# Kernel optimization log

Hardware: AMD Instinct MI355X
Metric: run time of the kernel (lower is better)

The kernel has to match this reference:

```python
import jax, jax.numpy as jnp
import numpy as np
from jax import lax

EPS = 1e-6


def layernorm2d(x, w, b):
    # channel LayerNorm over dim C of NCHW (biased variance), matching LayerNormFunction
    mu = jnp.mean(x, axis=1, keepdims=True)
    var = jnp.mean((x - mu) ** 2, axis=1, keepdims=True)
    y = (x - mu) * lax.rsqrt(var + EPS)
    return w[None, :, None, None] * y + b[None, :, None, None]


def conv1x1(x, W, b):
    # x: (N,C,H,W), W: (O,C), b: (O,)
    return jnp.einsum('nchw,oc->nohw', x, W) + b[None, :, None, None]


def conv3x3(x, W, b):
    # W: (O,I,3,3)
    y = lax.conv_general_dilated(x, W, window_strides=(1, 1), padding='SAME',
                                 dimension_numbers=('NCHW', 'OIHW', 'NCHW'))
    return y + b[None, :, None, None]


def avg_pool3x3(x):
    # torch F.avg_pool2d k=3, s=1, p=1, count_include_pad=True -> always divide by 9
    s = lax.reduce_window(x, 0.0, lax.add, (1, 1, 3, 3), (1, 1, 1, 1),
                          [(0, 0), (0, 0), (1, 1), (1, 1)])
    return s / 9.0


def setup_inputs() -> dict:
    key = jax.random.key(0)
    N, C, H, W = 8, 64, 128, 256
    ks = jax.random.split(key, 12)
    d = {
        'x_l': jax.random.normal(ks[0], (N, C, H, W), jnp.float32),
        'x_r': jax.random.normal(ks[1], (N, C, H, W), jnp.float32),
        'nl_w': jnp.ones((C,), jnp.float32),
        'nl_b': jnp.zeros((C,), jnp.float32),
        'nr_w': jnp.ones((C,), jnp.float32),
        'nr_b': jnp.zeros((C,), jnp.float32),
        'Wq_l': jax.random.normal(ks[2], (C, C), jnp.float32) * 0.05,
        'bq_l': jax.random.normal(ks[3], (C,), jnp.float32) * 0.05,
        'Wq_r': jax.random.normal(ks[4], (C, C), jnp.float32) * 0.05,
        'bq_r': jax.random.normal(ks[5], (C,), jnp.float32) * 0.05,
        'Wv_r': jax.random.normal(ks[6], (C, C), jnp.float32) * 0.05,
        'bv_r': jax.random.normal(ks[7], (C,), jnp.float32) * 0.05,
        'beta': jax.random.normal(ks[8], (1, C, 1, 1), jnp.float32) * 0.1,
        'gamma': jax.random.normal(ks[9], (1, C, 1, 1), jnp.float32) * 0.1,
        'W_hf': jax.random.normal(ks[10], (C, C, 3, 3), jnp.float32) * 0.02,
        'b_hf': jax.random.normal(ks[11], (C,), jnp.float32) * 0.02,
    }
    return d


def reference(x_l, x_r, nl_w, nl_b, nr_w, nr_b, Wq_l, bq_l, Wq_r, bq_r,
              Wv_r, bv_r, beta, gamma, W_hf, b_hf):
    C = x_l.shape[1]
    scale = C ** (-0.5)

    # Projections (1x1 convs); Q_l, Q_r, V_r as (N,H,W,C)
    Q_l = jnp.transpose(conv1x1(layernorm2d(x_l, nl_w, nl_b), Wq_l, bq_l), (0, 2, 3, 1))
    Q_r = jnp.transpose(conv1x1(layernorm2d(x_r, nr_w, nr_b), Wq_r, bq_r), (0, 2, 3, 1))
    V_r = jnp.transpose(conv1x1(x_r, Wv_r, bv_r), (0, 2, 3, 1))

    # Per-scanline cross attention: (N,H,W,W)
    attn = jnp.einsum('nhwc,nhvc->nhwv', Q_l, Q_r) * scale
    attn = jax.nn.softmax(attn, axis=-1)
    F_r2l = jnp.einsum('nhwv,nhvc->nhwc', attn, V_r)  # (N,H,W,C)
    F_r2l = jnp.transpose(F_r2l, (0, 3, 1, 2)) * beta  # (N,C,H,W)

    # High-frequency branch
    hf = conv3x3(x_r - avg_pool3x3(x_r), W_hf, b_hf)

    return x_l + F_r2l + gamma * hf
```

## Files before the change

### kernel.cpp

```cpp
#include <hip/hip_runtime.h>
#include <hip/hip_bf16.h>

#define N_ 8
#define C_ 64
#define H_ 128
#define W_ 256
#define HW_ (H_*W_)
#define CHW_ (C_*H_*W_)

typedef unsigned int u32;
typedef unsigned short u16;
typedef float f32x4 __attribute__((ext_vector_type(4)));
typedef short bf16x8 __attribute__((ext_vector_type(8)));

__device__ __forceinline__ float blo(u32 u) { return __uint_as_float(u << 16); }
__device__ __forceinline__ float bhi(u32 u) { return __uint_as_float(u & 0xffff0000u); }
__device__ __forceinline__ u16 f2bf(float f) {
    u32 u = __float_as_uint(f);
    u32 lsb = (u >> 16) & 1u;
    u += 0x7fffu + lsb;
    return (u16)(u >> 16);
}
__device__ __forceinline__ u32 pack2(float a, float b) {
    return (u32)f2bf(a) | ((u32)f2bf(b) << 16);
}
__device__ __forceinline__ int rmap(int px) {
    return (px & 0xF8) | ((px + (px >> 3)) & 7);
}

__global__ __launch_bounds__(512, 2) void k_fused(
    const float* __restrict__ xl, const float* __restrict__ xr,
    const float* __restrict__ nlw, const float* __restrict__ nlb,
    const float* __restrict__ nrw, const float* __restrict__ nrb,
    const float* __restrict__ Wql, const float* __restrict__ bql,
    const float* __restrict__ Wqr, const float* __restrict__ bqr,
    const float* __restrict__ Wvr, const float* __restrict__ bvr,
    const float* __restrict__ beta, float* __restrict__ out)
{
    __shared__ u32 B1[8192];
    __shared__ u32 B2[8192];
    __shared__ float muA[256], rsA[256];
    __shared__ float SlA[64], BlA[64], SrA[64], BrA[64], BvA[64];
    const int tid  = threadIdx.x;
    const int lane = tid & 63, wv = tid >> 6;
    const int l15  = lane & 15, kg = lane >> 4;
    const int mw   = wv & 3;
    const int nh   = wv >> 2;
    const int blk  = blockIdx.x;
    const int n = blk >> 7, h = blk & 127;
    const size_t gbase = (size_t)n*CHW_ + (size_t)h*W_;

    if (tid < 64) {
        const int o = tid;
        float sl = 0.f, bl = bql[o], sr = 0.f, br = bqr[o];
        for (int c = 0; c < 64; ++c) {
            float wl = Wql[o*64+c], wr = Wqr[o*64+c];
            sl += wl * nlw[c];
            bl += wl * nlb[c];
            sr += wr * nrw[c];
            br += wr * nrb[c];
        }
        SlA[o] = sl; BlA[o] = bl; SrA[o] = sr; BrA[o] = br; BvA[o] = bvr[o];
    }

    const int oA = mw*16 + l15;
    bf16x8 aL[2], aR[2], aV[2];
    #pragma unroll
    for (int hf = 0; hf < 2; ++hf) {
        bf16x8 tl, tr, tv;
        #pragma unroll
        for (int j = 0; j < 8; ++j) {
            const int c = hf*32 + kg*8 + j;
            tl[j] = (short)f2bf(Wql[oA*64+c] * nlw[c]);
            tr[j] = (short)f2bf(Wqr[oA*64+c] * nrw[c]);
            tv[j] = (short)f2bf(Wvr[oA*64+c]);
        }
        aL[hf] = tl; aR[hf] = tr; aV[hf] = tv;
    }

    {
        const int chunk = tid >> 6;
        const int j = tid & 63;
        const int c0 = chunk*8;
        float4 v[8];
        #pragma unroll
        for (int e = 0; e < 8; ++e)
            v[e] = *(const float4*)(xl + gbase + (size_t)(c0+e)*HW_ + j*4);
        #pragma unroll
        for (int t = 0; t < 4; ++t) {
            const int px = j*4 + t;
            const int r = rmap(px);
            u32 q0,q1,q2,q3;
            const float* f0 = (const float*)&v[0]; const float* f1 = (const float*)&v[1];
            const float* f2 = (const float*)&v[2]; const float* f3 = (const float*)&v[3];
            const float* f4 = (const float*)&v[4]; const float* f5 = (const float*)&v[5];
            const float* f6 = (const float*)&v[6]; const float* f7 = (const float*)&v[7];
            asm("v_cvt_pk_bf16_f32 %0, %1, %2" : "=v"(q0) : "v"(f0[t]), "v"(f1[t]));
            asm("v_cvt_pk_bf16_f32 %0, %1, %2" : "=v"(q1) : "v"(f2[t]), "v"(f3[t]));
            asm("v_cvt_pk_bf16_f32 %0, %1, %2" : "=v"(q2) : "v"(f4[t]), "v"(f5[t]));
            asm("v_cvt_pk_bf16_f32 %0, %1, %2" : "=v"(q3) : "v"(f6[t]), "v"(f7[t]));
            uint4 pv; pv.x=q0; pv.y=q1; pv.z=q2; pv.w=q3;
            *(uint4*)&B1[r*32 + ((chunk ^ (r&7))<<2)] = pv;
        }
    }
    __syncthreads();
    if (tid < 256) {
        const int px = tid;
        const int r = rmap(px);
        float sum = 0.f, ssq = 0.f;
        #pragma unroll
        for (int c8 = 0; c8 < 8; ++c8) {
            uint4 val = *(const uint4*)&B1[r*32 + ((c8 ^ (r&7))<<2)];
            const u32* wp = (const u32*)&val;
            #pragma unroll
            for (int q = 0; q < 4; ++q) {
                float a = blo(wp[q]), b = bhi(wp[q]);
                sum += a + b; ssq += a*a + b*b;
            }
        }
        float mu = sum * (1.f/64.f);
        float var = ssq * (1.f/64.f) - mu*mu;
        muA[px] = mu;
        rsA[px] = rsqrtf(var + 1e-6f);
    }
    __syncthreads();
    {
        float Sv[4], Bv[4];
        #pragma unroll
        for (int r4 = 0; r4 < 4; ++r4) {
            Sv[r4] = SlA[mw*16 + kg*4 + r4];
            Bv[r4] = BlA[mw*16 + kg*4 + r4];
        }
        #pragma unroll
        for (int nt2 = 0; nt2 < 8; ++nt2) {
            const int nt = nh*8 + nt2;
            const int px = nt*16 + l15;
            const int r = rmap(px);
            f32x4 d = {0.f,0.f,0.f,0.f};
            #pragma unroll
            for (int hf = 0; hf < 2; ++hf) {
                bf16x8 b = *(const bf16x8*)&B1[r*32 + (((hf*4+kg) ^ (r&7))<<2)];
                d = __builtin_amdgcn_mfma_f32_16x16x32_bf16(aL[hf], b, d, 0, 0, 0);
            }
            const float mu = muA[px], rs = rsA[px];
            uint2 pv;
            pv.x = pack2(rs*(d[0] - mu*Sv[0]) + Bv[0], rs*(d[1] - mu*Sv[1]) + Bv[1]);
            pv.y = pack2(rs*(d[2] - mu*Sv[2]) + Bv[2], rs*(d[3] - mu*Sv[3]) + Bv[3]);
            const int ci = (mw*2 + (kg>>1)) ^ (px & 7);
            *(uint2*)&B2[px*32 + (ci<<2) + (kg&1)*2] = pv;
        }
    }
    __syncthreads();

    bf16x8 qf[2][2];
    #pragma unroll
    for (int ntq = 0; ntq < 2; ++ntq)
        #pragma unroll
        for (int ci = 0; ci < 2; ++ci) {
            const int q = wv*32 + ntq*16 + l15;
            qf[ntq][ci] = *(const bf16x8*)&B2[q*32 + (((ci*4+kg) ^ (q&7))<<2)];
        }
    {
        const int chunk = tid >> 6;
        const int j = tid & 63;
        const int c0 = chunk*8;
        float4 v[8];
        #pragma unroll
        for (int e = 0; e < 8; ++e)
            v[e] = *(const float4*)(xr + gbase + (size_t)(c0+e)*HW_ + j*4);
        #pragma unroll
        for (int t = 0; t < 4; ++t) {
            const int px = j*4 + t;
            const int r = rmap(px);
            u32 q0,q1,q2,q3;
            const float* f0 = (const float*)&v[0]; const float* f1 = (const float*)&v[1];
            const float* f2 = (const float*)&v[2]; const float* f3 = (const float*)&v[3];
            const float* f4 = (const float*)&v[4]; const float* f5 = (const float*)&v[5];
            const float* f6 = (const float*)&v[6]; const float* f7 = (const float*)&v[7];
            asm("v_cvt_pk_bf16_f32 %0, %1, %2" : "=v"(q0) : "v"(f0[t]), "v"(f1[t]));
            asm("v_cvt_pk_bf16_f32 %0, %1, %2" : "=v"(q1) : "v"(f2[t]), "v"(f3[t]));
            asm("v_cvt_pk_bf16_f32 %0, %1, %2" : "=v"(q2) : "v"(f4[t]), "v"(f5[t]));
            asm("v_cvt_pk_bf16_f32 %0, %1, %2" : "=v"(q3) : "v"(f6[t]), "v"(f7[t]));
            uint4 pv; pv.x=q0; pv.y=q1; pv.z=q2; pv.w=q3;
            *(uint4*)&B1[r*32 + ((chunk ^ (r&7))<<2)] = pv;
        }
    }
    __syncthreads();
    if (tid < 256) {
        const int px = tid;
        const int r = rmap(px);
        float sum = 0.f, ssq = 0.f;
        #pragma unroll
        for (int c8 = 0; c8 < 8; ++c8) {
            uint4 val = *(const uint4*)&B1[r*32 + ((c8 ^ (r&7))<<2)];
            const u32* wp = (const u32*)&val;
            #pragma unroll
            for (int q = 0; q < 4; ++q) {
                float a = blo(wp[q]), b = bhi(wp[q]);
                sum += a + b; ssq += a*a + b*b;
            }
        }
        float mu = sum * (1.f/64.f);
        float var = ssq * (1.f/64.f) - mu*mu;
        muA[px] = mu;
        rsA[px] = rsqrtf(var + 1e-6f);
    }
    __syncthreads();

    u32 hq[8][2], hv[8][2];
    {
        float Sv[4], Bv[4];
        #pragma unroll
        for (int r4 = 0; r4 < 4; ++r4) {
            Sv[r4] = SrA[mw*16 + kg*4 + r4];
            Bv[r4] = BrA[mw*16 + kg*4 + r4];
        }
        const int chv = mw*16 + l15;
        const float vbias = BvA[chv];
        #pragma unroll
        for (int nt2 = 0; nt2 < 8; ++nt2) {
            const int nt = nh*8 + nt2;
            const int px = nt*16 + l15;
            const int r = rmap(px);
            bf16x8 bX[2];
            #pragma unroll
            for (int hf = 0; hf < 2; ++hf)
                bX[hf] = *(const bf16x8*)&B1[r*32 + (((hf*4+kg) ^ (r&7))<<2)];
            f32x4 dq = {0.f,0.f,0.f,0.f};
            f32x4 dv = {0.f,0.f,0.f,0.f};
            #pragma unroll
            for (int hf = 0; hf < 2; ++hf) {
                dq = __builtin_amdgcn_mfma_f32_16x16x32_bf16(aR[hf], bX[hf], dq, 0, 0, 0);
                dv = __builtin_amdgcn_mfma_f32_16x16x32_bf16(bX[hf], aV[hf], dv, 0, 0, 0);
            }
            const float mu = muA[px], rs = rsA[px];
            hq[nt2][0] = pack2(rs*(dq[0] - mu*Sv[0]) + Bv[0], rs*(dq[1] - mu*Sv[1]) + Bv[1]);
            hq[nt2][1] = pack2(rs*(dq[2] - mu*Sv[2]) + Bv[2], rs*(dq[3] - mu*Sv[3]) + Bv[3]);
            hv[nt2][0] = pack2(dv[0] + vbias, dv[1] + vbias);
            hv[nt2][1] = pack2(dv[2] + vbias, dv[3] + vbias);
        }
    }
    __syncthreads();
    {
        const int chv = mw*16 + l15;
        u16* Vts16 = (u16*)B2;
        #pragma unroll
        for (int nt2 = 0; nt2 < 8; ++nt2) {
            const int nt = nh*8 + nt2;
            const int px = nt*16 + l15;
            const int ciq = (mw*2 + (kg>>1)) ^ (px & 7);
            uint2 pq; pq.x = hq[nt2][0]; pq.y = hq[nt2][1];
            *(uint2*)&B1[px*32 + (ciq<<2) + (kg&1)*2] = pq;
            uint2 pw; pw.x = hv[nt2][0]; pw.y = hv[nt2][1];
            const int swz = (nt*2 + (kg>>1)) ^ (chv & 7);
            *(uint2*)&Vts16[chv*256 + (swz<<3) + (kg&1)*4] = pw;
        }
    }
    __syncthreads();

    f32x4 oacc[2][4];
    #pragma unroll
    for (int a = 0; a < 2; ++a)
        #pragma unroll
        for (int b = 0; b < 4; ++b)
            oacc[a][b] = (f32x4){0.f,0.f,0.f,0.f};
    float lsum[2] = {0.f,0.f};
    const uint4* KsR = (const uint4*)B1;
    const u16* Vts = (const u16*)B2;
    const int srcA = ((2*kg) & 3)*16 + l15;

    for (int kb = 0; kb < 8; ++kb) {
        f32x4 st[2][2];
        #pragma unroll
        for (int mt = 0; mt < 2; ++mt)
            #pragma unroll
            for (int nt = 0; nt < 2; ++nt)
                st[mt][nt] = (f32x4){0.f,0.f,0.f,0.f};
        #pragma unroll
        for (int ci = 0; ci < 2; ++ci) {
            bf16x8 a0 = *(const bf16x8*)&KsR[(kb*32 +      l15)*8 + ((ci*4 + kg) ^ (l15 & 7))];
            bf16x8 a1 = *(const bf16x8*)&KsR[(kb*32 + 16 + l15)*8 + ((ci*4 + kg) ^ (l15 & 7))];
            #pragma unroll
            for (int nt = 0; nt < 2; ++nt) {
                st[0][nt] = __builtin_amdgcn_mfma_f32_16x16x32_bf16(a0, qf[nt][ci], st[0][nt], 0, 0, 0);
                st[1][nt] = __builtin_amdgcn_mfma_f32_16x16x32_bf16(a1, qf[nt][ci], st[1][nt], 0, 0, 0);
            }
        }
        bf16x8 paR[2];
        #pragma unroll
        for (int nt = 0; nt < 2; ++nt) {
            float p00 = __expf(st[0][nt][0]*0.125f);
            float p01 = __expf(st[0][nt][1]*0.125f);
            float p02 = __expf(st[0][nt][2]*0.125f);
            float p03 = __expf(st[0][nt][3]*0.125f);
            float p10 = __expf(st[1][nt][0]*0.125f);
            float p11 = __expf(st[1][nt][1]*0.125f);
            float p12 = __expf(st[1][nt][2]*0.125f);
            float p13 = __expf(st[1][nt][3]*0.125f);
            lsum[nt] += ((p00+p01)+(p02+p03)) + ((p10+p11)+(p12+p13));
            u32 pk00, pk01, pk10, pk11;
            asm("v_cvt_pk_bf16_f32 %0, %1, %2" : "=v"(pk00) : "v"(p00), "v"(p01));
            asm("v_cvt_pk_bf16_f32 %0, %1, %2" : "=v"(pk01) : "v"(p02), "v"(p03));
            asm("v_cvt_pk_bf16_f32 %0, %1, %2" : "=v"(pk10) : "v"(p10), "v"(p11));
            asm("v_cvt_pk_bf16_f32 %0, %1, %2" : "=v"(pk11) : "v"(p12), "v"(p13));
            int a00 = __shfl((int)pk00, srcA, 64);
            int a01 = __shfl((int)pk01, srcA, 64);
            int a10 = __shfl((int)pk10, srcA, 64);
            int a11 = __shfl((int)pk11, srcA, 64);
            int b00 = __shfl((int)pk00, srcA + 16, 64);
            int b01 = __shfl((int)pk01, srcA + 16, 64);
            int b10 = __shfl((int)pk10, srcA + 16, 64);
            int b11 = __shfl((int)pk11, srcA + 16, 64);
            const bool lo = (kg < 2);
            union { u32 u[4]; bf16x8 v; } pu;
            pu.u[0] = (u32)(lo ? a00 : a10);
            pu.u[1] = (u32)(lo ? a01 : a11);
            pu.u[2] = (u32)(lo ? b00 : b10);
            pu.u[3] = (u32)(lo ? b01 : b11);
            paR[nt] = pu.v;
        }
        bf16x8 vb[4];
        #pragma unroll
        for (int nc = 0; nc < 4; ++nc)
            vb[nc] = *(const bf16x8*)&Vts[(nc*16 + l15)*256 + ((kb*4 + kg) ^ (l15 & 7))*8];
        #pragma unroll
        for (int qt = 0; qt < 2; ++qt)
            #pragma unroll
            for (int nc = 0; nc < 4; ++nc)
                oacc[qt][nc] = __builtin_amdgcn_mfma_f32_16x16x32_bf16(paR[qt], vb[nc], oacc[qt][nc], 0, 0, 0);
    }

    #pragma unroll
    for (int nt = 0; nt < 2; ++nt) {
        float s = lsum[nt];
        s += __shfl_xor(s, 16, 64);
        s += __shfl_xor(s, 32, 64);
        lsum[nt] = s;
    }
    float linv[2][4];
    #pragma unroll
    for (int qt = 0; qt < 2; ++qt)
        #pragma unroll
        for (int r = 0; r < 4; ++r)
            linv[qt][r] = 1.0f / __shfl(lsum[qt], kg*4 + r, 64);

    const size_t qbase = gbase + wv*32;
    #pragma unroll
    for (int nc = 0; nc < 4; ++nc) {
        const int ch = nc*16 + l15;
        const float bch = beta[ch];
        #pragma unroll
        for (int qt = 0; qt < 2; ++qt) {
            const size_t gidx = qbase + (size_t)ch*HW_ + qt*16 + kg*4;
            f32x4 x4 = *(const f32x4*)&xl[gidx];
            f32x4 vals;
            #pragma unroll
            for (int r = 0; r < 4; ++r)
                vals[r] = x4[r] + bch*(oacc[qt][nc][r]*linv[qt][r]);
            *(f32x4*)&out[gidx] = vals;
        }
    }
}

__global__ __launch_bounds__(256) void k_hipass(
    const float* __restrict__ xr, u16* __restrict__ Tt)
{
    __shared__ u16 Ts[64*256];
    const int bid = blockIdx.x;
    const int blk = (bid & 7)*128 + (bid >> 3);
    const int n = blk >> 7, h = blk & 127;
    const int tid = threadIdx.x;
    const int lane = tid & 63, wv = tid >> 6;
    const float* rowp = xr + (size_t)n*CHW_ + (size_t)h*W_ + lane*4;

    #pragma unroll
    for (int ci = 0; ci < 16; ++ci) {
        const int c = wv*16 + ci;
        const float* pc = rowp + (size_t)c*HW_;
        float ctr0=0.f, ctr1=0.f, ctr2=0.f, ctr3=0.f;
        float s0=0.f, s1=0.f, s2=0.f, s3=0.f;
        #pragma unroll
        for (int dy = -1; dy <= 1; ++dy) {
            const int hh = h + dy;
            float4 v = {0.f,0.f,0.f,0.f};
            if (hh >= 0 && hh < 128) v = *(const float4*)(pc + dy*W_);
            float lft = __shfl_up(v.w, 1);
            float rgt = __shfl_down(v.x, 1);
            if (lane == 0)  lft = 0.f;
            if (lane == 63) rgt = 0.f;
            s0 += lft + v.x + v.y;
            s1 += v.x + v.y + v.z;
            s2 += v.y + v.z + v.w;
            s3 += v.z + v.w + rgt;
            if (dy == 0) { ctr0=v.x; ctr1=v.y; ctr2=v.z; ctr3=v.w; }
        }
        uint2 pv;
        pv.x = pack2(ctr0 - s0*(1.f/9.f), ctr1 - s1*(1.f/9.f));
        pv.y = pack2(ctr2 - s2*(1.f/9.f), ctr3 - s3*(1.f/9.f));
        const int swz = (c >> 3) << 3;
        *(uint2*)&Ts[c*256 + ((lane*4) ^ swz)] = pv;
    }
    __syncthreads();
    uint4* gout = (uint4*)(Tt + (size_t)blk*256*64);
    #pragma unroll
    for (int iter = 0; iter < 8; ++iter) {
        const int lin = iter*256 + tid;
        const int px = lin >> 3, chunk = lin & 7;
        const int pxs = px ^ (chunk << 3);
        u32 w4[4];
        #pragma unroll
        for (int tp = 0; tp < 4; ++tp) {
            const int c0 = chunk*8 + tp*2;
            u16 a = Ts[(c0    )*256 + pxs];
            u16 b = Ts[(c0 + 1)*256 + pxs];
            w4[tp] = (u32)a | ((u32)b << 16);
        }
        uint4 v; v.x=w4[0]; v.y=w4[1]; v.z=w4[2]; v.w=w4[3];
        gout[lin] = v;
    }
}

__device__ __forceinline__ void conv_tile(
    const uint4* __restrict__ buf, const bf16x8* A,
    const float* gv, const float* bv,
    int n, int h, int w0, int mt, int l15, int kg,
    float* __restrict__ out)
{
    f32x4 acc[4] = {{0,0,0,0},{0,0,0,0},{0,0,0,0},{0,0,0,0}};
    #pragma unroll
    for (int s = 0; s < 18; ++s) {
        const int q  = s >> 1;
        const int dy = q / 3, dx = q % 3;
        const int c0 = (s & 1)*4 + kg;
        #pragma unroll
        for (int nt = 0; nt < 4; ++nt) {
            const int wt = nt*16 + l15 + dx;
            bf16x8 b = *(const bf16x8*)&buf[(dy*66 + wt)*8 + (c0 ^ (wt & 7))];
            acc[nt] = __builtin_amdgcn_mfma_f32_16x16x32_bf16(A[s], b, acc[nt], 0, 0, 0);
        }
    }
    #pragma unroll
    for (int nt = 0; nt < 4; ++nt) {
        const int px = w0 + nt*16 + l15;
        #pragma unroll
        for (int r = 0; r < 4; ++r) {
            const int oo = mt*16 + kg*4 + r;
            size_t idx = (size_t)(n*64 + oo)*HW_ + (size_t)h*W_ + px;
            out[idx] += gv[r]*(acc[nt][r] + bv[r]);
        }
    }
}

__global__ __launch_bounds__(256) void k_conv(
    const u16* __restrict__ Tt, const float* __restrict__ Whf,
    const float* __restrict__ bhf, const float* __restrict__ gam,
    float* __restrict__ out)
{
    __shared__ uint4 Xs[2][1584];
    const int tid  = threadIdx.x;
    const int lane = tid & 63;
    const int mt   = tid >> 6;
    const int l15  = lane & 15;
    const int kg   = lane >> 4;
    const int bid  = blockIdx.x;
    const int blk2 = (bid & 7)*256 + (bid >> 3);
    const int row  = blk2 >> 1, half = blk2 & 1;
    const int n = row >> 7, h = row & 127;
    const int w00 = half*128;
    const int w01 = w00 + 64;

    const int oa = mt*16 + l15;
    bf16x8 A[18];
    #pragma unroll
    for (int s = 0; s < 18; ++s) {
        const int q  = s >> 1;
        const int ib = (s & 1)*32 + kg*8;
        bf16x8 a;
        #pragma unroll
        for (int j = 0; j < 8; ++j) {
            float wv = Whf[(size_t)(oa*64 + ib + j)*9 + q];
            a[j] = (short)f2bf(wv);
        }
        A[s] = a;
    }
    float gv[4], bv[4];
    #pragma unroll
    for (int r = 0; r < 4; ++r) {
        int oo = mt*16 + kg*4 + r;
        gv[r] = gam[oo];
        bv[r] = bhf[oo];
    }

    for (int it = tid; it < 1584; it += 256) {
        int dy    = it / 528;
        int rem   = it - dy*528;
        int wt    = rem >> 3;
        int chunk = rem & 7;
        int hh = h + dy - 1;
        int wg = w00 + wt - 1;
        uint4 v = {0,0,0,0};
        if (hh >= 0 && hh < 128 && wg >= 0 && wg < 256)
            v = *(const uint4*)(Tt + (((size_t)(n*128 + hh)*256 + wg)*64 + chunk*8));
        Xs[0][(dy*66 + wt)*8 + (chunk ^ (wt & 7))] = v;
    }
    __syncthreads();

    uint4 rr[7];
    #pragma unroll
    for (int k = 0; k < 7; ++k) {
        const int it = k*256 + tid;
        if (it < 1584) {
            int dy    = it / 528;
            int rem   = it - dy*528;
            int wt    = rem >> 3;
            int chunk = rem & 7;
            int hh = h + dy - 1;
            int wg = w01 + wt - 1;
            uint4 v = {0,0,0,0};
            if (hh >= 0 && hh < 128 && wg >= 0 && wg < 256)
                v = *(const uint4*)(Tt + (((size_t)(n*128 + hh)*256 + wg)*64 + chunk*8));
            rr[k] = v;
        }
    }

    conv_tile(&Xs[0][0], A, gv, bv, n, h, w00, mt, l15, kg, out);

    #pragma unroll
    for (int k = 0; k < 7; ++k) {
        const int it = k*256 + tid;
        if (it < 1584) {
            int dy    = it / 528;
            int rem   = it - dy*528;
            int wt    = rem >> 3;
            int chunk = rem & 7;
            Xs[1][(dy*66 + wt)*8 + (chunk ^ (wt & 7))] = rr[k];
        }
    }
    __syncthreads();
    conv_tile(&Xs[1][0], A, gv, bv, n, h, w01, mt, l15, kg, out);
}

extern "C" void kernel_launch(void* const* d_in, const int* in_sizes, int n_in,
                              void* d_out, int out_size, void* d_ws, size_t ws_size,
                              hipStream_t stream)
{
    const float* xl   = (const float*)d_in[0];
    const float* xr   = (const float*)d_in[1];
    const float* nlw  = (const float*)d_in[2];
    const float* nlb  = (const float*)d_in[3];
    const float* nrw  = (const float*)d_in[4];
    const float* nrb  = (const float*)d_in[5];
    const float* Wql  = (const float*)d_in[6];
    const float* bql  = (const float*)d_in[7];
    const float* Wqr  = (const float*)d_in[8];
    const float* bqr  = (const float*)d_in[9];
    const float* Wvr  = (const float*)d_in[10];
    const float* bvr  = (const float*)d_in[11];
    const float* beta = (const float*)d_in[12];
    const float* gam  = (const float*)d_in[13];
    const float* Whf  = (const float*)d_in[14];
    const float* bhf  = (const float*)d_in[15];
    float* out = (float*)d_out;

    u16* Tt = (u16*)d_ws;

    k_hipass<<<1024, 256, 0, stream>>>(xr, Tt);
    k_fused<<<1024, 512, 0, stream>>>(xl, xr, nlw, nlb, nrw, nrb,
                                      Wql, bql, Wqr, bqr, Wvr, bvr,
                                      beta, out);
    k_conv<<<2048, 256, 0, stream>>>(Tt, Whf, bhf, gam, out);
}
```

Baseline: 176.7 us.

## Prefetch x_r before LayerNorm barrier and move x_l residual add into conv kernel

The fused attention kernel now issues the x_r global loads before the first LayerNorm barrier, so they overlap the x_l normalization work instead of stalling later. The x_l residual is no longer read in the attention epilogue. It is added in the conv epilogue, which already reads and writes out. Total x_l traffic stays the same, but the load moves to the conv kernel's scattered epilogue access pattern, and holding the prefetched values raises register pressure in the fused kernel.

```diff
diff --git a/kernel.cpp b/kernel.cpp
--- a/kernel.cpp
+++ b/kernel.cpp
@@ -78,17 +78,18 @@
         aL[hf] = tl; aR[hf] = tr; aV[hf] = tv;
     }
 
+    const int schunk = tid >> 6;
+    const int sj     = tid & 63;
+
     {
-        const int chunk = tid >> 6;
-        const int j = tid & 63;
-        const int c0 = chunk*8;
+        const int c0 = schunk*8;
         float4 v[8];
         #pragma unroll
         for (int e = 0; e < 8; ++e)
-            v[e] = *(const float4*)(xl + gbase + (size_t)(c0+e)*HW_ + j*4);
+            v[e] = *(const float4*)(xl + gbase + (size_t)(c0+e)*HW_ + sj*4);
         #pragma unroll
         for (int t = 0; t < 4; ++t) {
-            const int px = j*4 + t;
+            const int px = sj*4 + t;
             const int r = rmap(px);
             u32 q0,q1,q2,q3;
             const float* f0 = (const float*)&v[0]; const float* f1 = (const float*)&v[1];
@@ -100,8 +101,15 @@
             asm("v_cvt_pk_bf16_f32 %0, %1, %2" : "=v"(q2) : "v"(f4[t]), "v"(f5[t]));
             asm("v_cvt_pk_bf16_f32 %0, %1, %2" : "=v"(q3) : "v"(f6[t]), "v"(f7[t]));
             uint4 pv; pv.x=q0; pv.y=q1; pv.z=q2; pv.w=q3;
-            *(uint4*)&B1[r*32 + ((chunk ^ (r&7))<<2)] = pv;
-        }
+            *(uint4*)&B1[r*32 + ((schunk ^ (r&7))<<2)] = pv;
+        }
+    }
+    float4 vr2[8];
+    {
+        const int c0 = schunk*8;
+        #pragma unroll
+        for (int e = 0; e < 8; ++e)
+            vr2[e] = *(const float4*)(xr + gbase + (size_t)(c0+e)*HW_ + sj*4);
     }
     __syncthreads();
     if (tid < 256) {
@@ -161,28 +169,21 @@
             qf[ntq][ci] = *(const bf16x8*)&B2[q*32 + (((ci*4+kg) ^ (q&7))<<2)];
         }
     {
-        const int chunk = tid >> 6;
-        const int j = tid & 63;
-        const int c0 = chunk*8;
-        float4 v[8];
-        #pragma unroll
-        for (int e = 0; e < 8; ++e)
-            v[e] = *(const float4*)(xr + gbase + (size_t)(c0+e)*HW_ + j*4);
         #pragma unroll
         for (int t = 0; t < 4; ++t) {
-            const int px = j*4 + t;
+            const int px = sj*4 + t;
             const int r = rmap(px);
             u32 q0,q1,q2,q3;
-            const float* f0 = (const float*)&v[0]; const float* f1 = (const float*)&v[1];
-            const float* f2 = (const float*)&v[2]; const float* f3 = (const float*)&v[3];
-            const float* f4 = (const float*)&v[4]; const float* f5 = (const float*)&v[5];
-            const float* f6 = (const float*)&v[6]; const float* f7 = (const float*)&v[7];
+            const float* f0 = (const float*)&vr2[0]; const float* f1 = (const float*)&vr2[1];
+            const float* f2 = (const float*)&vr2[2]; const float* f3 = (const float*)&vr2[3];
+            const float* f4 = (const float*)&vr2[4]; const float* f5 = (const float*)&vr2[5];
+            const float* f6 = (const float*)&vr2[6]; const float* f7 = (const float*)&vr2[7];
             asm("v_cvt_pk_bf16_f32 %0, %1, %2" : "=v"(q0) : "v"(f0[t]), "v"(f1[t]));
             asm("v_cvt_pk_bf16_f32 %0, %1, %2" : "=v"(q1) : "v"(f2[t]), "v"(f3[t]));
             asm("v_cvt_pk_bf16_f32 %0, %1, %2" : "=v"(q2) : "v"(f4[t]), "v"(f5[t]));
             asm("v_cvt_pk_bf16_f32 %0, %1, %2" : "=v"(q3) : "v"(f6[t]), "v"(f7[t]));
             uint4 pv; pv.x=q0; pv.y=q1; pv.z=q2; pv.w=q3;
-            *(uint4*)&B1[r*32 + ((chunk ^ (r&7))<<2)] = pv;
+            *(uint4*)&B1[r*32 + ((schunk ^ (r&7))<<2)] = pv;
         }
     }
     __syncthreads();
@@ -352,11 +353,10 @@
         #pragma unroll
         for (int qt = 0; qt < 2; ++qt) {
             const size_t gidx = qbase + (size_t)ch*HW_ + qt*16 + kg*4;
-            f32x4 x4 = *(const f32x4*)&xl[gidx];
             f32x4 vals;
             #pragma unroll
             for (int r = 0; r < 4; ++r)
-                vals[r] = x4[r] + bch*(oacc[qt][nc][r]*linv[qt][r]);
+                vals[r] = bch*(oacc[qt][nc][r]*linv[qt][r]);
             *(f32x4*)&out[gidx] = vals;
         }
     }
@@ -424,7 +424,7 @@
     const uint4* __restrict__ buf, const bf16x8* A,
     const float* gv, const float* bv,
     int n, int h, int w0, int mt, int l15, int kg,
-    float* __restrict__ out)
+    const float* __restrict__ xl, float* __restrict__ out)
 {
     f32x4 acc[4] = {{0,0,0,0},{0,0,0,0},{0,0,0,0},{0,0,0,0}};
     #pragma unroll
@@ -446,7 +446,7 @@
         for (int r = 0; r < 4; ++r) {
             const int oo = mt*16 + kg*4 + r;
             size_t idx = (size_t)(n*64 + oo)*HW_ + (size_t)h*W_ + px;
-            out[idx] += gv[r]*(acc[nt][r] + bv[r]);
+            out[idx] = out[idx] + xl[idx] + gv[r]*(acc[nt][r] + bv[r]);
         }
     }
 }
@@ -454,7 +454,7 @@
 __global__ __launch_bounds__(256) void k_conv(
     const u16* __restrict__ Tt, const float* __restrict__ Whf,
     const float* __restrict__ bhf, const float* __restrict__ gam,
-    float* __restrict__ out)
+    const float* __restrict__ xl, float* __restrict__ out)
 {
     __shared__ uint4 Xs[2][1584];
     const int tid  = threadIdx.x;
@@ -523,7 +523,7 @@
         }
     }
 
-    conv_tile(&Xs[0][0], A, gv, bv, n, h, w00, mt, l15, kg, out);
+    conv_tile(&Xs[0][0], A, gv, bv, n, h, w00, mt, l15, kg, xl, out);
 
     #pragma unroll
     for (int k = 0; k < 7; ++k) {
@@ -537,7 +537,7 @@
         }
     }
     __syncthreads();
-    conv_tile(&Xs[1][0], A, gv, bv, n, h, w01, mt, l15, kg, out);
+    conv_tile(&Xs[1][0], A, gv, bv, n, h, w01, mt, l15, kg, xl, out);
 }
 
 extern "C" void kernel_launch(void* const* d_in, const int* in_sizes, int n_in,
@@ -568,5 +568,5 @@
     k_fused<<<1024, 512, 0, stream>>>(xl, xr, nlw, nlb, nrw, nrb,
                                       Wql, bql, Wqr, bqr, Wvr, bvr,
                                       beta, out);
-    k_conv<<<2048, 256, 0, stream>>>(Tt, Whf, bhf, gam, out);
-}
+    k_conv<<<2048, 256, 0, stream>>>(Tt, Whf, bhf, gam, xl, out);
+}
```

New measurement: 193.8 us. +9.7%, slower.
